# Optimization experiments

Hardware: AMD Instinct MI355X
Metric: run time of the kernel (lower is better)

## Reference

```python
import jax, jax.numpy as jnp
import numpy as np

N_NODES = 100000
N_EDGES = 1600000
IN_DIM, HID_DIM, OUT_DIM = 128, 128, 64


def setup_inputs() -> dict:
    key = jax.random.key(0)
    ks = jax.random.split(key, 5)
    x = jax.random.normal(ks[0], (N_NODES, IN_DIM), dtype=jnp.float32)
    edge_index = jax.random.randint(ks[1], (2, N_EDGES), 0, N_NODES, dtype=jnp.int64)
    W1 = jax.random.normal(ks[2], (IN_DIM, HID_DIM), dtype=jnp.float32) * (1.0 / np.sqrt(IN_DIM))
    b1 = jnp.zeros((HID_DIM,), dtype=jnp.float32)
    W2 = jax.random.normal(ks[3], (HID_DIM, OUT_DIM), dtype=jnp.float32) * (1.0 / np.sqrt(HID_DIM))
    b2 = jnp.zeros((OUT_DIM,), dtype=jnp.float32)
    return {"x": x, "edge_index": edge_index, "W1": W1, "b1": b1, "W2": W2, "b2": b2}


def _gcn_conv(h, row, col, norm, b, n_nodes):
    # h: [N, F] already linearly transformed; message = norm_e * h[src]; scatter-add to dst
    msg = h[row] * norm[:, None]                      # [E+N, F]
    out = jax.ops.segment_sum(msg, col, num_segments=n_nodes)
    return out + b


def reference(x, edge_index, W1, b1, W2, b2):
    n = x.shape[0]
    loops = jnp.arange(n, dtype=edge_index.dtype)
    row = jnp.concatenate([edge_index[0], loops])     # sources (incl. self loops)
    col = jnp.concatenate([edge_index[1], loops])     # targets
    # symmetric normalization: deg over targets with unit edge weights
    deg = jax.ops.segment_sum(jnp.ones_like(col, dtype=x.dtype), col, num_segments=n)
    dinv = jnp.where(deg > 0, jax.lax.rsqrt(jnp.maximum(deg, 1.0)), 0.0)
    norm = dinv[row] * dinv[col]                      # [E+N]
    h = jax.nn.relu(_gcn_conv(x @ W1, row, col, norm, b1, n))
    out = _gcn_conv(h @ W2, row, col, norm, b2, n)
    return out.mean(axis=0)                           # [OUT_DIM]
```

## Files before the change

### kernel.cpp

```cpp
#include <hip/hip_runtime.h>

#define N_NODES 100000
#define N_EDGES 1600000
#define IN_DIM 128
#define HID_DIM 128
#define OUT_DIM 64
#define BKT_SHIFT 8
#define BKT_SIZE 256
#define NBKT ((N_NODES + BKT_SIZE - 1) / BKT_SIZE)
#define B1 256
#define HIST_N (NBKT * B1)
#define HIST_N2 (2 * HIST_N)
#define GEMM_BLKS ((N_NODES + 127) / 128)

typedef float v2f __attribute__((ext_vector_type(2)));
typedef float v4f __attribute__((ext_vector_type(4)));
typedef short v8s __attribute__((ext_vector_type(8)));

__device__ __forceinline__ unsigned int f2bf(float f) {
  unsigned int u = __float_as_uint(f);
  return (u + 0x7FFFu + ((u >> 16) & 1u)) >> 16;
}

template <bool HI>
__device__ __forceinline__ v2f cvt8(unsigned int u) {
  return __builtin_amdgcn_cvt_pk_f32_fp8((int)u, HI);
}

__device__ __forceinline__ float wdec(unsigned int p) {
  return __uint_as_float((p >> 17) << 16);
}

__device__ __forceinline__ void load4(const void* ei, int is64, int half, int base,
                                      int* v) {
  if (is64) {
    const long long* e = (const long long*)ei + (size_t)half * N_EDGES + base;
    longlong2 a = *(const longlong2*)e;
    longlong2 b = *(const longlong2*)(e + 2);
    v[0] = (int)a.x; v[1] = (int)a.y; v[2] = (int)b.x; v[3] = (int)b.y;
  } else {
    const int* e = (const int*)ei + (size_t)half * N_EDGES + base;
    int4 a = *(const int4*)e;
    v[0] = a.x; v[1] = a.y; v[2] = a.z; v[3] = a.w;
  }
}

__device__ __forceinline__ int detect64_block(const unsigned int* ei, int* sh) {
  if (threadIdx.x == 0) *sh = 0;
  __syncthreads();
  if (ei[1 + 2 * threadIdx.x] != 0u) *sh = 1;
  __syncthreads();
  return (*sh == 0) ? 1 : 0;
}

__global__ __launch_bounds__(256) void front_kernel(const float* __restrict__ x,
                                                    const float* __restrict__ W,
                                                    const void* ei,
                                                    unsigned int* __restrict__ G,
                                                    int* hist, float* S) {
  __shared__ __align__(16) char smem[2 * 128 * 136 * 2];
  if (blockIdx.x >= GEMM_BLKS) {
    int* hd = (int*)smem;
    int* hs = hd + NBKT;
    int* sh = hs + NBKT;
    const int hb = blockIdx.x - GEMM_BLKS;
    if (hb == 0 && threadIdx.x < HID_DIM) S[threadIdx.x] = 0.f;
    const int is64 = detect64_block((const unsigned int*)ei, sh);
    for (int k = threadIdx.x; k < NBKT; k += 256) { hd[k] = 0; hs[k] = 0; }
    __syncthreads();
    for (int g = hb * 256 + threadIdx.x; g < N_EDGES / 4; g += B1 * 256) {
      int r[4], c[4];
      load4(ei, is64, 0, g * 4, r);
      load4(ei, is64, 1, g * 4, c);
#pragma unroll
      for (int k = 0; k < 4; k++) {
        atomicAdd(&hd[c[k] >> BKT_SHIFT], 1);
        atomicAdd(&hs[r[k] >> BKT_SHIFT], 1);
      }
    }
    __syncthreads();
    for (int k = threadIdx.x; k < NBKT; k += 256) {
      hist[k * B1 + hb] = hd[k];
      hist[HIST_N + k * B1 + hb] = hs[k];
    }
    return;
  }
  typedef unsigned short us_row[136];
  us_row* lx = (us_row*)smem;
  us_row* lwt = (us_row*)(smem + 128 * 136 * 2);
  const int t = threadIdx.x;
  const int row0 = blockIdx.x * 128;

  {
    const float4* W4 = (const float4*)W;
    for (int it = 0; it < 16; ++it) {
      int idx = t + 256 * it;
      int k = idx >> 5, c4 = (idx & 31) * 4;
      float4 w = W4[idx];
      lwt[c4 + 0][k] = (unsigned short)f2bf(w.x);
      lwt[c4 + 1][k] = (unsigned short)f2bf(w.y);
      lwt[c4 + 2][k] = (unsigned short)f2bf(w.z);
      lwt[c4 + 3][k] = (unsigned short)f2bf(w.w);
    }
  }
  {
    const float4* x4 = (const float4*)(x + (size_t)row0 * IN_DIM);
    for (int it = 0; it < 16; ++it) {
      int idx = t + 256 * it;
      int r = idx >> 5, kq = (idx & 31) * 4;
      float4 v = make_float4(0.f, 0.f, 0.f, 0.f);
      if (row0 + r < N_NODES) v = x4[idx];
      unsigned int p0 = (f2bf(v.y) << 16) | f2bf(v.x);
      unsigned int p1 = (f2bf(v.w) << 16) | f2bf(v.z);
      *(uint2*)&lx[r][kq] = make_uint2(p0, p1);
    }
  }
  __syncthreads();

  const int lane = t & 63;
  const int wv = t >> 6;
  const int m0 = wv * 32;
  const int lrow = lane & 15;
  const int lk = (lane >> 4) * 8;

  v4f acc[2][8];
#pragma unroll
  for (int si = 0; si < 2; si++)
#pragma unroll
    for (int n = 0; n < 8; n++) acc[si][n] = (v4f){0.f, 0.f, 0.f, 0.f};

#pragma unroll
  for (int kk = 0; kk < 128; kk += 32) {
    v8s a0 = *(const v8s*)&lx[m0 + lrow][kk + lk];
    v8s a1 = *(const v8s*)&lx[m0 + 16 + lrow][kk + lk];
#pragma unroll
    for (int n = 0; n < 8; n++) {
      v8s b = *(const v8s*)&lwt[n * 16 + lrow][kk + lk];
      acc[0][n] = __builtin_amdgcn_mfma_f32_16x16x32_bf16(a0, b, acc[0][n], 0, 0, 0);
      acc[1][n] = __builtin_amdgcn_mfma_f32_16x16x32_bf16(a1, b, acc[1][n], 0, 0, 0);
    }
  }

  unsigned char* G8 = (unsigned char*)G;
#pragma unroll
  for (int si = 0; si < 2; si++)
#pragma unroll
    for (int n = 0; n < 8; n++) {
      int colg = n * 16 + (lane & 15);
#pragma unroll
      for (int i = 0; i < 4; i++) {
        int r = row0 + m0 + si * 16 + (lane >> 4) * 4 + i;
        if (r < N_NODES) {
          float v = acc[si][n][i];
          int pk = __builtin_amdgcn_cvt_pk_fp8_f32(v, v, 0, false);
          G8[(size_t)r * HID_DIM + colg] = (unsigned char)(pk & 0xFF);
        }
      }
    }
}

__global__ void scan1_kernel(int* arr, int* bsum, int n) {
  __shared__ int tmp[256];
  int i = blockIdx.x * 256 + threadIdx.x;
  int v = (i < n) ? arr[i] : 0;
  tmp[threadIdx.x] = v;
  __syncthreads();
  for (int off = 1; off < 256; off <<= 1) {
    int t2 = (threadIdx.x >= off) ? tmp[threadIdx.x - off] : 0;
    __syncthreads();
    tmp[threadIdx.x] += t2;
    __syncthreads();
  }
  if (i < n) arr[i] = tmp[threadIdx.x] - v;
  if (threadIdx.x == 255) bsum[blockIdx.x] = tmp[255];
}

__global__ void scan2_kernel(int* bsum, int nb) {
  __shared__ int tmp[1024];
  int v = (threadIdx.x < nb) ? bsum[threadIdx.x] : 0;
  tmp[threadIdx.x] = v;
  __syncthreads();
  for (int off = 1; off < 1024; off <<= 1) {
    int t2 = (threadIdx.x >= off) ? tmp[threadIdx.x - off] : 0;
    __syncthreads();
    tmp[threadIdx.x] += t2;
    __syncthreads();
  }
  if (threadIdx.x < nb) bsum[threadIdx.x] = tmp[threadIdx.x] - v;
}

__global__ __launch_bounds__(256) void scatter_kernel(const void* ei, const int* hist,
                                                      const int* bsum,
                                                      unsigned int* pairs) {
  __shared__ int cd[NBKT], cs[NBKT], sh[1];
  const int is64 = detect64_block((const unsigned int*)ei, sh);
  for (int k = threadIdx.x; k < NBKT; k += 256) {
    cd[k] = hist[k * B1 + blockIdx.x] + bsum[k];
    cs[k] = hist[HIST_N + k * B1 + blockIdx.x] + bsum[NBKT + k];
  }
  __syncthreads();
  for (int g = blockIdx.x * 256 + threadIdx.x; g < N_EDGES / 4; g += B1 * 256) {
    int r[4], c[4];
    load4(ei, is64, 0, g * 4, r);
    load4(ei, is64, 1, g * 4, c);
#pragma unroll
    for (int k = 0; k < 4; k++) {
      int pd = atomicAdd(&cd[c[k] >> BKT_SHIFT], 1);
      pairs[pd] = ((unsigned int)(c[k] & (BKT_SIZE - 1)) << 17) | (unsigned int)r[k];
      int ps = atomicAdd(&cs[r[k] >> BKT_SHIFT], 1);
      pairs[ps] = ((unsigned int)(r[k] & (BKT_SIZE - 1)) << 17) | (unsigned int)c[k];
    }
  }
}

__global__ __launch_bounds__(256) void csr_kernel(const int* hist, const int* bsum,
                                                  const unsigned int* pairs,
                                                  int* rowptr, unsigned int* csr,
                                                  float* dinv) {
  __shared__ int cnt[BKT_SIZE], sc[BKT_SIZE], cur[BKT_SIZE];
  const int k = blockIdx.x;
  const int base = hist[k * B1] + bsum[k];
  const int end = (k == NBKT - 1) ? N_EDGES : hist[(k + 1) * B1] + bsum[k + 1];
  const int nseg = end - base;
  const int l = threadIdx.x;
  cnt[l] = 0;
  __syncthreads();
  for (int i = l; i < nseg; i += 256) atomicAdd(&cnt[pairs[base + i] >> 17], 1);
  __syncthreads();
  sc[l] = cnt[l];
  __syncthreads();
  for (int off = 1; off < BKT_SIZE; off <<= 1) {
    int v = (l >= off) ? sc[l - off] : 0;
    __syncthreads();
    sc[l] += v;
    __syncthreads();
  }
  {
    int excl = sc[l] - cnt[l];
    cur[l] = base + excl;
    int v = k * BKT_SIZE + l;
    if (v < N_NODES) {
      rowptr[v] = base + excl;
      dinv[v] = rsqrtf((float)(cnt[l] + 1));
    }
  }
  if (k == NBKT - 1 && l == 0) rowptr[N_NODES] = N_EDGES;
  __syncthreads();
  for (int i = l; i < nseg; i += 256) {
    unsigned int pk = pairs[base + i];
    int pos = atomicAdd(&cur[pk >> 17], 1);
    csr[pos] = pk & 0x1FFFFu;
  }
}

__global__ __launch_bounds__(256) void outsum_kernel(const int* hist, const int* bsum,
                                                     const unsigned int* pairs,
                                                     const float* __restrict__ dinv,
                                                     float* wacc,
                                                     unsigned int* __restrict__ csr) {
  __shared__ float fb[BKT_SIZE];
  const int k = blockIdx.x;
  const int base = hist[HIST_N + k * B1] + bsum[NBKT + k];
  const int end =
      (k == NBKT - 1) ? 2 * N_EDGES : hist[HIST_N + (k + 1) * B1] + bsum[NBKT + k + 1];
  fb[threadIdx.x] = 0.f;
  __syncthreads();
  for (int i = base + threadIdx.x; i < end; i += 256) {
    unsigned int pk = pairs[i];
    atomicAdd(&fb[pk >> 17], dinv[pk & 0x1FFFFu]);
  }
  for (int i = blockIdx.x * 256 + threadIdx.x; i < N_EDGES; i += NBKT * 256) {
    unsigned int src = __builtin_nontemporal_load(&csr[i]) & 0x1FFFFu;
    unsigned int bits = f2bf(dinv[src]);
    __builtin_nontemporal_store((bits << 17) | src, &csr[i]);
  }
  __syncthreads();
  int v = k * BKT_SIZE + threadIdx.x;
  if (v < N_NODES) wacc[v] = fb[threadIdx.x];
}

__global__ __launch_bounds__(256) void aggregate_kernel(
    const unsigned int* __restrict__ G, const int* __restrict__ rowptr,
    const unsigned int* __restrict__ csr, const float* __restrict__ dinv,
    const float* __restrict__ wacc, const float* __restrict__ b1,
    float* __restrict__ S) {
  const int lane = threadIdx.x & 63;
  const int sub = lane & 31;
  const int half = lane >> 5;
  const int wid = blockIdx.x * 4 + (threadIdx.x >> 6);
  const int nwaves = gridDim.x * 4;
  const float4 b = ((const float4*)b1)[sub];
  v2f s01 = {0.f, 0.f}, s23 = {0.f, 0.f};

  for (int c = wid; c < N_NODES; c += nwaves) {
    const int start = rowptr[c];
    const int cnum = rowptr[c + 1] - start;
    const float d = dinv[c];
    v2f a01 = {0.f, 0.f}, a23 = {0.f, 0.f};
    if (half == 0) {
      unsigned int g = G[c * 32 + sub];
      a01 = cvt8<false>(g) * d;
      a23 = cvt8<true>(g) * d;
    }
    for (int j0 = 0; j0 < cnum; j0 += 64) {
      unsigned int pkl = 0;
      if (j0 + lane < cnum)
        pkl = __builtin_nontemporal_load(&csr[start + j0 + lane]);
      const int m = min(64, cnum - j0);
      int i = 0;
      for (; i + 8 <= m; i += 8) {
        unsigned int p0 = __shfl(pkl, i + half);
        unsigned int p1 = __shfl(pkl, i + 2 + half);
        unsigned int p2 = __shfl(pkl, i + 4 + half);
        unsigned int p3 = __shfl(pkl, i + 6 + half);
        unsigned int g0 = G[(p0 & 0x1FFFFu) * 32 + sub];
        unsigned int g1 = G[(p1 & 0x1FFFFu) * 32 + sub];
        unsigned int g2 = G[(p2 & 0x1FFFFu) * 32 + sub];
        unsigned int g3 = G[(p3 & 0x1FFFFu) * 32 + sub];
        float w0 = wdec(p0), w1 = wdec(p1), w2 = wdec(p2), w3 = wdec(p3);
        a01 += cvt8<false>(g0) * w0; a23 += cvt8<true>(g0) * w0;
        a01 += cvt8<false>(g1) * w1; a23 += cvt8<true>(g1) * w1;
        a01 += cvt8<false>(g2) * w2; a23 += cvt8<true>(g2) * w2;
        a01 += cvt8<false>(g3) * w3; a23 += cvt8<true>(g3) * w3;
      }
      for (; i + 2 <= m; i += 2) {
        unsigned int p = __shfl(pkl, i + half);
        unsigned int g = G[(p & 0x1FFFFu) * 32 + sub];
        float w = wdec(p);
        a01 += cvt8<false>(g) * w;
        a23 += cvt8<true>(g) * w;
      }
      if (i < m) {
        unsigned int p = __shfl(pkl, i);
        if (half == 0) {
          unsigned int g = G[(p & 0x1FFFFu) * 32 + sub];
          float w = wdec(p);
          a01 += cvt8<false>(g) * w;
          a23 += cvt8<true>(g) * w;
        }
      }
    }
    a01.x += __shfl(a01.x, sub + 32);
    a01.y += __shfl(a01.y, sub + 32);
    a23.x += __shfl(a23.x, sub + 32);
    a23.y += __shfl(a23.y, sub + 32);
    if (half == 0) {
      float wc = d * (wacc[c] + d);
      s01.x += wc * fmaxf(fmaf(d, a01.x, b.x), 0.f);
      s01.y += wc * fmaxf(fmaf(d, a01.y, b.y), 0.f);
      s23.x += wc * fmaxf(fmaf(d, a23.x, b.z), 0.f);
      s23.y += wc * fmaxf(fmaf(d, a23.y, b.w), 0.f);
    }
  }

  __shared__ float ls[HID_DIM];
  if (threadIdx.x < HID_DIM) ls[threadIdx.x] = 0.f;
  __syncthreads();
  if (half == 0) {
    atomicAdd(&ls[4 * sub + 0], s01.x);
    atomicAdd(&ls[4 * sub + 1], s01.y);
    atomicAdd(&ls[4 * sub + 2], s23.x);
    atomicAdd(&ls[4 * sub + 3], s23.y);
  }
  __syncthreads();
  if (threadIdx.x < HID_DIM) atomicAdd(&S[threadIdx.x], ls[threadIdx.x]);
}

__global__ void finish_kernel(const float* __restrict__ S, const float* __restrict__ W2,
                              const float* __restrict__ b2, float* __restrict__ out) {
  int j = threadIdx.x;
  float acc = 0.f;
  for (int k = 0; k < HID_DIM; k++) acc += S[k] * W2[k * OUT_DIM + j];
  out[j] = acc * (1.0f / N_NODES) + b2[j];
}

extern "C" void kernel_launch(void* const* d_in, const int* in_sizes, int n_in,
                              void* d_out, int out_size, void* d_ws, size_t ws_size,
                              hipStream_t stream) {
  const float* x  = (const float*)d_in[0];
  const void*  ei = d_in[1];
  const float* W1 = (const float*)d_in[2];
  const float* b1 = (const float*)d_in[3];
  const float* W2 = (const float*)d_in[4];
  const float* b2 = (const float*)d_in[5];
  float* out = (float*)d_out;

  char* p = (char*)d_ws;
  size_t off = 0;
  auto alloc = [&](size_t bytes) -> void* {
    void* r = p + off;
    off = (off + bytes + 63) & ~(size_t)63;
    return r;
  };
  int*   hist   = (int*)alloc((size_t)HIST_N2 * 4);
  int*   bsum   = (int*)alloc(1024 * 4);
  unsigned int* pairs = (unsigned int*)alloc((size_t)2 * N_EDGES * 4);
  int*   rowptr = (int*)alloc(((size_t)N_NODES + 1) * 4);
  unsigned int* csr = (unsigned int*)alloc((size_t)N_EDGES * 4);
  float* dinv   = (float*)alloc((size_t)N_NODES * 4);
  float* wacc   = (float*)alloc((size_t)N_NODES * 4);
  float* S      = (float*)alloc(HID_DIM * 4);
  unsigned int* G = (unsigned int*)alloc((size_t)N_NODES * HID_DIM);
  (void)ws_size; (void)n_in; (void)in_sizes; (void)out_size;

  const int NBH = HIST_N2 / 256;

  front_kernel<<<GEMM_BLKS + B1, 256, 0, stream>>>(x, W1, ei, G, hist, S);
  scan1_kernel<<<NBH, 256, 0, stream>>>(hist, bsum, HIST_N2);
  scan2_kernel<<<1, 1024, 0, stream>>>(bsum, NBH);
  scatter_kernel<<<B1, 256, 0, stream>>>(ei, hist, bsum, pairs);
  csr_kernel<<<NBKT, 256, 0, stream>>>(hist, bsum, pairs, rowptr, csr, dinv);
  outsum_kernel<<<NBKT, 256, 0, stream>>>(hist, bsum, pairs, dinv, wacc, csr);
  aggregate_kernel<<<2048, 256, 0, stream>>>(G, rowptr, csr, dinv, wacc, b1, S);
  finish_kernel<<<1, 64, 0, stream>>>(S, W2, b2, out);
}
```

Baseline: 288.1 us.

## Split CSR build into count and fill, fusing bf16 dinv packing into the fill

Halves the bucket size to 128 nodes, doubling the number of buckets and blocks and reducing per-block shared atomic contention. The CSR kernel is split into a counting/rowptr/dinv pass and a fill pass. Because dinv is now known before the fill, the fill pass writes the bf16-packed dinv directly instead of re-reading and rewriting csr in a separate loop. The fill pass and the out-degree weight sum are merged into one launch, and scan2 is widened to two elements per thread to handle the larger histogram. In exchange this adds a launch boundary and gives more, smaller blocks in which half the threads sit idle during the per-bucket scans.

New measurement: 291.6 us. No clear change (+1.2%).

```diff
diff --git a/kernel.cpp b/kernel.cpp
--- a/kernel.cpp
+++ b/kernel.cpp
@@ -5,8 +5,8 @@
 #define IN_DIM 128
 #define HID_DIM 128
 #define OUT_DIM 64
-#define BKT_SHIFT 8
-#define BKT_SIZE 256
+#define BKT_SHIFT 7
+#define BKT_SIZE 128
 #define NBKT ((N_NODES + BKT_SIZE - 1) / BKT_SIZE)
 #define B1 256
 #define HIST_N (NBKT * B1)
@@ -177,16 +177,21 @@
 
 __global__ void scan2_kernel(int* bsum, int nb) {
   __shared__ int tmp[1024];
-  int v = (threadIdx.x < nb) ? bsum[threadIdx.x] : 0;
-  tmp[threadIdx.x] = v;
+  const int t = threadIdx.x;
+  int v0 = (2 * t < nb) ? bsum[2 * t] : 0;
+  int v1 = (2 * t + 1 < nb) ? bsum[2 * t + 1] : 0;
+  int s = v0 + v1;
+  tmp[t] = s;
   __syncthreads();
   for (int off = 1; off < 1024; off <<= 1) {
-    int t2 = (threadIdx.x >= off) ? tmp[threadIdx.x - off] : 0;
-    __syncthreads();
-    tmp[threadIdx.x] += t2;
-    __syncthreads();
-  }
-  if (threadIdx.x < nb) bsum[threadIdx.x] = tmp[threadIdx.x] - v;
+    int t2 = (t >= off) ? tmp[t - off] : 0;
+    __syncthreads();
+    tmp[t] += t2;
+    __syncthreads();
+  }
+  int excl = tmp[t] - s;
+  if (2 * t < nb) bsum[2 * t] = excl;
+  if (2 * t + 1 < nb) bsum[2 * t + 1] = excl + v0;
 }
 
 __global__ __launch_bounds__(256) void scatter_kernel(const void* ei, const int* hist,
@@ -213,31 +218,29 @@
   }
 }
 
-__global__ __launch_bounds__(256) void csr_kernel(const int* hist, const int* bsum,
-                                                  const unsigned int* pairs,
-                                                  int* rowptr, unsigned int* csr,
-                                                  float* dinv) {
-  __shared__ int cnt[BKT_SIZE], sc[BKT_SIZE], cur[BKT_SIZE];
+__global__ __launch_bounds__(256) void csrA_kernel(const int* hist, const int* bsum,
+                                                   const unsigned int* pairs,
+                                                   int* rowptr, float* dinv) {
+  __shared__ int cnt[BKT_SIZE], sc[BKT_SIZE];
   const int k = blockIdx.x;
   const int base = hist[k * B1] + bsum[k];
   const int end = (k == NBKT - 1) ? N_EDGES : hist[(k + 1) * B1] + bsum[k + 1];
   const int nseg = end - base;
   const int l = threadIdx.x;
-  cnt[l] = 0;
+  if (l < BKT_SIZE) cnt[l] = 0;
   __syncthreads();
   for (int i = l; i < nseg; i += 256) atomicAdd(&cnt[pairs[base + i] >> 17], 1);
   __syncthreads();
-  sc[l] = cnt[l];
+  if (l < BKT_SIZE) sc[l] = cnt[l];
   __syncthreads();
   for (int off = 1; off < BKT_SIZE; off <<= 1) {
-    int v = (l >= off) ? sc[l - off] : 0;
-    __syncthreads();
-    sc[l] += v;
-    __syncthreads();
-  }
-  {
+    int v = (l < BKT_SIZE && l >= off) ? sc[l - off] : 0;
+    __syncthreads();
+    if (l < BKT_SIZE) sc[l] += v;
+    __syncthreads();
+  }
+  if (l < BKT_SIZE) {
     int excl = sc[l] - cnt[l];
-    cur[l] = base + excl;
     int v = k * BKT_SIZE + l;
     if (v < N_NODES) {
       rowptr[v] = base + excl;
@@ -245,38 +248,49 @@
     }
   }
   if (k == NBKT - 1 && l == 0) rowptr[N_NODES] = N_EDGES;
-  __syncthreads();
-  for (int i = l; i < nseg; i += 256) {
-    unsigned int pk = pairs[base + i];
-    int pos = atomicAdd(&cur[pk >> 17], 1);
-    csr[pos] = pk & 0x1FFFFu;
-  }
-}
-
-__global__ __launch_bounds__(256) void outsum_kernel(const int* hist, const int* bsum,
-                                                     const unsigned int* pairs,
-                                                     const float* __restrict__ dinv,
-                                                     float* wacc,
-                                                     unsigned int* __restrict__ csr) {
+}
+
+__global__ __launch_bounds__(256) void csrBout_kernel(const int* hist, const int* bsum,
+                                                      const unsigned int* pairs,
+                                                      const int* __restrict__ rowptr,
+                                                      const float* __restrict__ dinv,
+                                                      unsigned int* __restrict__ csr,
+                                                      float* __restrict__ wacc) {
+  if (blockIdx.x < NBKT) {
+    __shared__ int cur[BKT_SIZE];
+    const int k = blockIdx.x;
+    const int base = hist[k * B1] + bsum[k];
+    const int end = (k == NBKT - 1) ? N_EDGES : hist[(k + 1) * B1] + bsum[k + 1];
+    const int nseg = end - base;
+    const int l = threadIdx.x;
+    if (l < BKT_SIZE) {
+      int v = k * BKT_SIZE + l;
+      cur[l] = (v < N_NODES) ? rowptr[v] : 0;
+    }
+    __syncthreads();
+    for (int i = l; i < nseg; i += 256) {
+      unsigned int pk = pairs[base + i];
+      unsigned int src = pk & 0x1FFFFu;
+      int pos = atomicAdd(&cur[pk >> 17], 1);
+      unsigned int bits = f2bf(dinv[src]);
+      csr[pos] = (bits << 17) | src;
+    }
+    return;
+  }
   __shared__ float fb[BKT_SIZE];
-  const int k = blockIdx.x;
+  const int k = blockIdx.x - NBKT;
   const int base = hist[HIST_N + k * B1] + bsum[NBKT + k];
   const int end =
       (k == NBKT - 1) ? 2 * N_EDGES : hist[HIST_N + (k + 1) * B1] + bsum[NBKT + k + 1];
-  fb[threadIdx.x] = 0.f;
+  if (threadIdx.x < BKT_SIZE) fb[threadIdx.x] = 0.f;
   __syncthreads();
   for (int i = base + threadIdx.x; i < end; i += 256) {
     unsigned int pk = pairs[i];
     atomicAdd(&fb[pk >> 17], dinv[pk & 0x1FFFFu]);
   }
-  for (int i = blockIdx.x * 256 + threadIdx.x; i < N_EDGES; i += NBKT * 256) {
-    unsigned int src = __builtin_nontemporal_load(&csr[i]) & 0x1FFFFu;
-    unsigned int bits = f2bf(dinv[src]);
-    __builtin_nontemporal_store((bits << 17) | src, &csr[i]);
-  }
   __syncthreads();
   int v = k * BKT_SIZE + threadIdx.x;
-  if (v < N_NODES) wacc[v] = fb[threadIdx.x];
+  if (threadIdx.x < BKT_SIZE && v < N_NODES) wacc[v] = fb[threadIdx.x];
 }
 
 __global__ __launch_bounds__(256) void aggregate_kernel(
@@ -393,7 +407,7 @@
     return r;
   };
   int*   hist   = (int*)alloc((size_t)HIST_N2 * 4);
-  int*   bsum   = (int*)alloc(1024 * 4);
+  int*   bsum   = (int*)alloc(2048 * 4);
   unsigned int* pairs = (unsigned int*)alloc((size_t)2 * N_EDGES * 4);
   int*   rowptr = (int*)alloc(((size_t)N_NODES + 1) * 4);
   unsigned int* csr = (unsigned int*)alloc((size_t)N_EDGES * 4);
@@ -409,8 +423,9 @@
   scan1_kernel<<<NBH, 256, 0, stream>>>(hist, bsum, HIST_N2);
   scan2_kernel<<<1, 1024, 0, stream>>>(bsum, NBH);
   scatter_kernel<<<B1, 256, 0, stream>>>(ei, hist, bsum, pairs);
-  csr_kernel<<<NBKT, 256, 0, stream>>>(hist, bsum, pairs, rowptr, csr, dinv);
-  outsum_kernel<<<NBKT, 256, 0, stream>>>(hist, bsum, pairs, dinv, wacc, csr);
+  csrA_kernel<<<NBKT, 256, 0, stream>>>(hist, bsum, pairs, rowptr, dinv);
+  csrBout_kernel<<<2 * NBKT, 256, 0, stream>>>(hist, bsum, pairs, rowptr, dinv, csr,
+                                               wacc);
   aggregate_kernel<<<2048, 256, 0, stream>>>(G, rowptr, csr, dinv, wacc, b1, S);
   finish_kernel<<<1, 64, 0, stream>>>(S, W2, b2, out);
 }
```
